# Performance work log

Hardware: AMD Instinct MI355X
Metric: run time of the kernel (lower is better)

The kernel has to match this reference:

```python
import jax, jax.numpy as jnp
import numpy as np

# SqueezeSeg CRF config
NUM_CLASS = 4
SIZE_Z, SIZE_A = 3, 5            # LCN_HEIGHT, LCN_WIDTH
B, H, W = 16, 64, 512            # batch, zenith, azimuth
RCRF_ITER = 3
BI_FILTER_COEF = 0.1
ANG_FILTER_COEF = 0.02
ANG_THETA_A = 0.9
BILATERAL_THETA_A = 0.9
K = SIZE_Z * SIZE_A              # 15 -> 14 neighbors (center excluded)

# neighbor offsets of the 3x5 condensing kernel, center excluded
OFFSETS = [(dz, da) for dz in range(SIZE_Z) for da in range(SIZE_A)
           if not (dz == SIZE_Z // 2 and da == SIZE_A // 2)]

def _gauss_weights(theta_sq):
    # angular_filter_kernel: Gaussian of squared spatial offset, center zeroed
    g = [np.exp(-((dz - SIZE_Z // 2) ** 2 + (da - SIZE_A // 2) ** 2) / (2.0 * theta_sq))
         for dz, da in OFFSETS]
    return jnp.asarray(np.array(g, dtype=np.float32))

def gather_neighbors(x):
    # x: [B,C,H,W] -> [B,C,K-1,H,W]; zero-padded 'same' neighborhood gather
    pz, pa = SIZE_Z // 2, SIZE_A // 2
    xp = jnp.pad(x, ((0, 0), (0, 0), (pz, pz), (pa, pa)))
    return jnp.stack([xp[:, :, dz:dz + H, da:da + W] for dz, da in OFFSETS], axis=2)

def setup_inputs() -> dict:
    key = jax.random.key(0)
    k1, k2, k3 = jax.random.split(key, 3)
    x = jax.random.normal(k1, (B, NUM_CLASS, H, W), dtype=jnp.float32)
    bilateral_filters = jax.random.uniform(k2, (B, 1, K - 1, H, W), dtype=jnp.float32)
    lidar_mask = (jax.random.uniform(k3, (B, 1, H, W)) > 0.5).astype(jnp.float32)
    return {"x": x, "bilateral_filters": bilateral_filters, "lidar_mask": lidar_mask}

def reference(x, bilateral_filters, lidar_mask):
    g_ang = _gauss_weights(ANG_THETA_A ** 2)
    g_bi = _gauss_weights(BILATERAL_THETA_A ** 2)
    compat = jnp.ones((NUM_CLASS, NUM_CLASS), jnp.float32) - jnp.eye(NUM_CLASS, dtype=jnp.float32)
    ang_compat = compat * ANG_FILTER_COEF   # [out_class, in_class] 1x1 conv
    bi_compat = compat * BI_FILTER_COEF

    for _ in range(RCRF_ITER):
        unary = jax.nn.softmax(x, axis=1)                     # softmax over class dim
        nb = gather_neighbors(unary)                          # [B,C,14,H,W]
        # depthwise angular filters = Gaussian-weighted neighbor sums
        ang = jnp.einsum('k,bckhw->bchw', g_ang, nb)
        bi_ang = jnp.einsum('k,bckhw->bchw', g_bi, nb)
        # condensing conv on masked unary, weighted by per-pixel bilateral filters
        nb_m = gather_neighbors(unary * lidar_mask)           # [B,C,14,H,W]
        condensed = jnp.sum(nb_m * bilateral_filters, axis=2) # [B,C,H,W]
        bi = condensed * lidar_mask * bi_ang
        # 1x1 compatibility transforms
        ang2 = jnp.einsum('oc,bchw->bohw', ang_compat, ang)
        bi2 = jnp.einsum('oc,bchw->bohw', bi_compat, bi)
        x = unary + ang2 + bi2
    return x
```

## Files before the change

kernel.cpp:

```cpp
#include <hip/hip_runtime.h>


#define NCLASS 4
#define HH 64
#define WW 512
#define BB 16
#define TH 8
#define TW 64
#define UR (TH + 6)
#define UC (TW + 12)
#define PLANE (HH * WW)

#define G1 0.53940412f
#define G2 0.29095687f
#define G4 0.08466190f
#define G5 0.04566227f

#define TAPS                                                                 \
    const int   DZ[14] = {-1,-1,-1,-1,-1,  0, 0, 0, 0,  1, 1, 1, 1, 1};      \
    const int   DA[14] = {-2,-1, 0, 1, 2, -2,-1, 1, 2, -2,-1, 0, 1, 2};      \
    const float GW[14] = {G5,G2,G1,G2,G5, G4,G1,G1,G4, G5,G2,G1,G2,G5};

template <int MR, int MC, bool FINAL>
__device__ __forceinline__ void crf_step(
    float4 (*__restrict__ u_lds)[UC], const float (*__restrict__ m_lds)[UC],
    const float* __restrict__ filt, float* __restrict__ dst,
    int b, int h0, int w0, int tid)
{
    constexpr int RH = TH + 2 * MR;
    constexpr int RW = TW + 2 * MC;
    constexpr int NS = (RH * RW + 255) / 256;
    TAPS

    float4 xnew[NS];

#pragma unroll
    for (int j = 0; j < NS; ++j) {
        const int s = tid + 256 * j;
        float4 r = make_float4(0.f, 0.f, 0.f, 0.f);
        if (s < RH * RW) {
            const int lr = s / RW;
            const int lc = s - lr * RW;
            const int gh = h0 + lr - MR;
            const int gw = w0 + lc - MC;
            const int ur = lr + (3 - MR);
            const int uc = lc + (6 - MC);
            if (gh >= 0 && gh < HH && gw >= 0 && gw < WW) {
                float a0 = 0.f, a1 = 0.f, a2 = 0.f, a3 = 0.f;
                float c0 = 0.f, c1 = 0.f, c2 = 0.f, c3 = 0.f;
                const float mcen = m_lds[ur][uc];
                const float* fp = filt + ((size_t)b * 14 * HH + gh) * WW + gw;
#pragma unroll
                for (int k = 0; k < 14; ++k) {
                    const float  f  = fp[(size_t)k * PLANE];
                    const float  mn = m_lds[ur + DZ[k]][uc + DA[k]];
                    const float4 u  = u_lds[ur + DZ[k]][uc + DA[k]];
                    const float  fm = f * mn;
                    const float  gk = GW[k];
                    a0 = fmaf(gk, u.x, a0);  c0 = fmaf(fm, u.x, c0);
                    a1 = fmaf(gk, u.y, a1);  c1 = fmaf(fm, u.y, c1);
                    a2 = fmaf(gk, u.z, a2);  c2 = fmaf(fm, u.z, c2);
                    a3 = fmaf(gk, u.w, a3);  c3 = fmaf(fm, u.w, c3);
                }
                const float b0 = c0 * mcen * a0;
                const float b1 = c1 * mcen * a1;
                const float b2 = c2 * mcen * a2;
                const float b3 = c3 * mcen * a3;
                const float sa = a0 + a1 + a2 + a3;
                const float sb = b0 + b1 + b2 + b3;
                const float4 ucen = u_lds[ur][uc];
                r.x = ucen.x + 0.02f * (sa - a0) + 0.1f * (sb - b0);
                r.y = ucen.y + 0.02f * (sa - a1) + 0.1f * (sb - b1);
                r.z = ucen.z + 0.02f * (sa - a2) + 0.1f * (sb - b2);
                r.w = ucen.w + 0.02f * (sa - a3) + 0.1f * (sb - b3);
                if (!FINAL) {
                    const float mx  = fmaxf(fmaxf(r.x, r.y), fmaxf(r.z, r.w));
                    const float e0  = __expf(r.x - mx);
                    const float e1  = __expf(r.y - mx);
                    const float e2  = __expf(r.z - mx);
                    const float e3  = __expf(r.w - mx);
                    const float inv = 1.0f / (e0 + e1 + e2 + e3);
                    r = make_float4(e0 * inv, e1 * inv, e2 * inv, e3 * inv);
                }
            }
            if (FINAL) {
                float* o = dst + ((size_t)b * NCLASS * HH + gh) * WW + gw;
                o[0]         = r.x;
                o[PLANE]     = r.y;
                o[2 * PLANE] = r.z;
                o[3 * PLANE] = r.w;
            }
        }
        if (!FINAL) xnew[j] = r;
    }

    if (!FINAL) {
        __syncthreads();
#pragma unroll
        for (int j = 0; j < NS; ++j) {
            const int s = tid + 256 * j;
            if (s < RH * RW) {
                const int lr = s / RW;
                const int lc = s - lr * RW;
                u_lds[lr + (3 - MR)][lc + (6 - MC)] = xnew[j];
            }
        }
        __syncthreads();
    }
}

__global__ __launch_bounds__(256, 4) void crf_fused(
    const float* __restrict__ xin,
    const float* __restrict__ filt,
    const float* __restrict__ mask,
    float* __restrict__ xout)
{
    __shared__ float4 u_lds[UR][UC];
    __shared__ float  m_lds[UR][UC];

    const int b   = blockIdx.z;
    const int h0  = blockIdx.y * TH;
    const int w0  = blockIdx.x * TW;
    const int tid = threadIdx.x;

    for (int idx = tid; idx < UR * UC; idx += 256) {
        const int lr = idx / UC;
        const int lc = idx - lr * UC;
        const int gh = h0 + lr - 3;
        const int gw = w0 + lc - 6;
        float4 u = make_float4(0.f, 0.f, 0.f, 0.f);
        float  m = 0.f;
        if (gh >= 0 && gh < HH && gw >= 0 && gw < WW) {
            const float* px = xin + ((size_t)b * NCLASS * HH + gh) * WW + gw;
            const float v0 = px[0];
            const float v1 = px[PLANE];
            const float v2 = px[2 * PLANE];
            const float v3 = px[3 * PLANE];
            const float mx = fmaxf(fmaxf(v0, v1), fmaxf(v2, v3));
            const float e0 = __expf(v0 - mx);
            const float e1 = __expf(v1 - mx);
            const float e2 = __expf(v2 - mx);
            const float e3 = __expf(v3 - mx);
            const float inv = 1.0f / (e0 + e1 + e2 + e3);
            u = make_float4(e0 * inv, e1 * inv, e2 * inv, e3 * inv);
            m = mask[((size_t)b * HH + gh) * WW + gw];
        }
        u_lds[lr][lc] = u;
        m_lds[lr][lc] = m;
    }
    __syncthreads();

    crf_step<2, 4, false>(u_lds, m_lds, filt, xout, b, h0, w0, tid);
    crf_step<1, 2, false>(u_lds, m_lds, filt, xout, b, h0, w0, tid);
    crf_step<0, 0, true >(u_lds, m_lds, filt, xout, b, h0, w0, tid);
}

extern "C" void kernel_launch(void* const* d_in, const int* in_sizes, int n_in,
                              void* d_out, int out_size, void* d_ws, size_t ws_size,
                              hipStream_t stream) {
    const float* x    = (const float*)d_in[0];
    const float* filt = (const float*)d_in[1];
    const float* msk  = (const float*)d_in[2];
    float* out = (float*)d_out;
    (void)d_ws; (void)ws_size;

    dim3 grid(WW / TW, HH / TH, BB);
    dim3 block(256);
    crf_fused<<<grid, block, 0, stream>>>(x, filt, msk, out);
}
```

Measured before the change: 98.66 us.

## Process two adjacent pixels per thread with swizzled LDS and vectorized loads

Each thread now computes two horizontally adjacent pixels. Each stencil row of six LDS values is loaded once and shared by both outputs, which reduces LDS reads per pixel. The bilateral filter, input and mask loads and the output stores become float2 accesses. LDS columns are swizzled (even/odd split) so that threads reading pairs avoid bank conflicts. The cost is higher register pressure from the 28 filter values and doubled accumulators, which may reduce occupancy, and odd-width halo regions need extra edge-handling branches.

```diff
diff --git a/kernel.cpp b/kernel.cpp
--- a/kernel.cpp
+++ b/kernel.cpp
@@ -9,6 +9,7 @@
 #define TW 64
 #define UR (TH + 6)
 #define UC (TW + 12)
+#define UCH (UC / 2)
 #define PLANE (HH * WW)
 
 #define G1 0.53940412f
@@ -16,10 +17,24 @@
 #define G4 0.08466190f
 #define G5 0.04566227f
 
-#define TAPS                                                                 \
-    const int   DZ[14] = {-1,-1,-1,-1,-1,  0, 0, 0, 0,  1, 1, 1, 1, 1};      \
-    const int   DA[14] = {-2,-1, 0, 1, 2, -2,-1, 1, 2, -2,-1, 0, 1, 2};      \
-    const float GW[14] = {G5,G2,G1,G2,G5, G4,G1,G1,G4, G5,G2,G1,G2,G5};
+__device__ __forceinline__ constexpr int swz(int c) {
+    return (c & 1) * UCH + (c >> 1);
+}
+
+__device__ __forceinline__ constexpr int tapk(int dz, int da) {
+    const int idx = (dz + 1) * 5 + (da + 2);
+    return idx > 7 ? idx - 1 : idx;
+}
+
+__device__ __forceinline__ float4 softmax4(float4 v) {
+    const float mx = fmaxf(fmaxf(v.x, v.y), fmaxf(v.z, v.w));
+    const float e0 = __expf(v.x - mx);
+    const float e1 = __expf(v.y - mx);
+    const float e2 = __expf(v.z - mx);
+    const float e3 = __expf(v.w - mx);
+    const float inv = 1.0f / (e0 + e1 + e2 + e3);
+    return make_float4(e0 * inv, e1 * inv, e2 * inv, e3 * inv);
+}
 
 template <int MR, int MC, bool FINAL>
 __device__ __forceinline__ void crf_step(
@@ -27,82 +42,143 @@
     const float* __restrict__ filt, float* __restrict__ dst,
     int b, int h0, int w0, int tid)
 {
-    constexpr int RH = TH + 2 * MR;
-    constexpr int RW = TW + 2 * MC;
-    constexpr int NS = (RH * RW + 255) / 256;
-    TAPS
-
-    float4 xnew[NS];
+    constexpr int RH  = TH + 2 * MR;
+    constexpr int RW  = TW + 2 * MC;
+    constexpr int NPX = RH * RW;
+    constexpr int NS  = (NPX + 511) / 512;
+    const float GW[14] = {G5,G2,G1,G2,G5, G4,G1,G1,G4, G5,G2,G1,G2,G5};
+
+    float4 xn[NS][2];
 
 #pragma unroll
     for (int j = 0; j < NS; ++j) {
-        const int s = tid + 256 * j;
-        float4 r = make_float4(0.f, 0.f, 0.f, 0.f);
-        if (s < RH * RW) {
+        xn[j][0] = make_float4(0.f, 0.f, 0.f, 0.f);
+        xn[j][1] = make_float4(0.f, 0.f, 0.f, 0.f);
+        const int s = 2 * (tid + 256 * j);
+        if (s < NPX) {
             const int lr = s / RW;
             const int lc = s - lr * RW;
             const int gh = h0 + lr - MR;
             const int gw = w0 + lc - MC;
             const int ur = lr + (3 - MR);
             const int uc = lc + (6 - MC);
-            if (gh >= 0 && gh < HH && gw >= 0 && gw < WW) {
-                float a0 = 0.f, a1 = 0.f, a2 = 0.f, a3 = 0.f;
-                float c0 = 0.f, c1 = 0.f, c2 = 0.f, c3 = 0.f;
-                const float mcen = m_lds[ur][uc];
-                const float* fp = filt + ((size_t)b * 14 * HH + gh) * WW + gw;
+            const bool rowIn = (gh >= 0) && (gh < HH);
+            const bool in0 = rowIn && (gw >= 0) && (gw < WW);
+            const bool in1 = rowIn && (gw + 1 >= 0) && (gw + 1 < WW);
+
+            float F0[14], F1[14];
+            const float* fp = filt + ((size_t)b * 14 * HH + gh) * WW + gw;
+            if (in0 && in1) {
 #pragma unroll
                 for (int k = 0; k < 14; ++k) {
-                    const float  f  = fp[(size_t)k * PLANE];
-                    const float  mn = m_lds[ur + DZ[k]][uc + DA[k]];
-                    const float4 u  = u_lds[ur + DZ[k]][uc + DA[k]];
-                    const float  fm = f * mn;
-                    const float  gk = GW[k];
-                    a0 = fmaf(gk, u.x, a0);  c0 = fmaf(fm, u.x, c0);
-                    a1 = fmaf(gk, u.y, a1);  c1 = fmaf(fm, u.y, c1);
-                    a2 = fmaf(gk, u.z, a2);  c2 = fmaf(fm, u.z, c2);
-                    a3 = fmaf(gk, u.w, a3);  c3 = fmaf(fm, u.w, c3);
-                }
-                const float b0 = c0 * mcen * a0;
-                const float b1 = c1 * mcen * a1;
-                const float b2 = c2 * mcen * a2;
-                const float b3 = c3 * mcen * a3;
-                const float sa = a0 + a1 + a2 + a3;
-                const float sb = b0 + b1 + b2 + b3;
-                const float4 ucen = u_lds[ur][uc];
-                r.x = ucen.x + 0.02f * (sa - a0) + 0.1f * (sb - b0);
-                r.y = ucen.y + 0.02f * (sa - a1) + 0.1f * (sb - b1);
-                r.z = ucen.z + 0.02f * (sa - a2) + 0.1f * (sb - b2);
-                r.w = ucen.w + 0.02f * (sa - a3) + 0.1f * (sb - b3);
-                if (!FINAL) {
-                    const float mx  = fmaxf(fmaxf(r.x, r.y), fmaxf(r.z, r.w));
-                    const float e0  = __expf(r.x - mx);
-                    const float e1  = __expf(r.y - mx);
-                    const float e2  = __expf(r.z - mx);
-                    const float e3  = __expf(r.w - mx);
-                    const float inv = 1.0f / (e0 + e1 + e2 + e3);
-                    r = make_float4(e0 * inv, e1 * inv, e2 * inv, e3 * inv);
-                }
-            }
+                    const float2 f2 = *(const float2*)(fp + (size_t)k * PLANE);
+                    F0[k] = f2.x; F1[k] = f2.y;
+                }
+            } else {
+#pragma unroll
+                for (int k = 0; k < 14; ++k) {
+                    F0[k] = in0 ? fp[(size_t)k * PLANE] : 0.f;
+                    F1[k] = in1 ? fp[(size_t)k * PLANE + 1] : 0.f;
+                }
+            }
+
+            float4 A0 = make_float4(0.f,0.f,0.f,0.f), C0 = A0, A1 = A0, C1 = A0;
+            float4 cen0, cen1;
+            float  mc0 = 0.f, mc1 = 0.f;
+#pragma unroll
+            for (int dz = -1; dz <= 1; ++dz) {
+                const int rr = ur + dz;
+                float4 U[6];
+                float  M[6];
+#pragma unroll
+                for (int t = 0; t < 6; ++t) {
+                    const int col = uc - 2 + t;
+                    U[t] = u_lds[rr][swz(col)];
+                    M[t] = m_lds[rr][swz(col)];
+                }
+                if (dz == 0) {
+                    cen0 = U[2]; cen1 = U[3];
+                    mc0  = M[2]; mc1  = M[3];
+                }
+#pragma unroll
+                for (int da = -2; da <= 2; ++da) {
+                    if (dz == 0 && da == 0) continue;
+                    const int   k   = tapk(dz, da);
+                    const float gk  = GW[k];
+                    const float fm0 = F0[k] * M[da + 2];
+                    const float fm1 = F1[k] * M[da + 3];
+                    const float4 u0 = U[da + 2];
+                    const float4 u1 = U[da + 3];
+                    A0.x = fmaf(gk,  u0.x, A0.x);  C0.x = fmaf(fm0, u0.x, C0.x);
+                    A0.y = fmaf(gk,  u0.y, A0.y);  C0.y = fmaf(fm0, u0.y, C0.y);
+                    A0.z = fmaf(gk,  u0.z, A0.z);  C0.z = fmaf(fm0, u0.z, C0.z);
+                    A0.w = fmaf(gk,  u0.w, A0.w);  C0.w = fmaf(fm0, u0.w, C0.w);
+                    A1.x = fmaf(gk,  u1.x, A1.x);  C1.x = fmaf(fm1, u1.x, C1.x);
+                    A1.y = fmaf(gk,  u1.y, A1.y);  C1.y = fmaf(fm1, u1.y, C1.y);
+                    A1.z = fmaf(gk,  u1.z, A1.z);  C1.z = fmaf(fm1, u1.z, C1.z);
+                    A1.w = fmaf(gk,  u1.w, A1.w);  C1.w = fmaf(fm1, u1.w, C1.w);
+                }
+            }
+
+            const float b0x = C0.x * mc0 * A0.x;
+            const float b0y = C0.y * mc0 * A0.y;
+            const float b0z = C0.z * mc0 * A0.z;
+            const float b0w = C0.w * mc0 * A0.w;
+            const float b1x = C1.x * mc1 * A1.x;
+            const float b1y = C1.y * mc1 * A1.y;
+            const float b1z = C1.z * mc1 * A1.z;
+            const float b1w = C1.w * mc1 * A1.w;
+            const float sa0 = A0.x + A0.y + A0.z + A0.w;
+            const float sb0 = b0x + b0y + b0z + b0w;
+            const float sa1 = A1.x + A1.y + A1.z + A1.w;
+            const float sb1 = b1x + b1y + b1z + b1w;
+            float4 r0, r1;
+            r0.x = cen0.x + 0.02f * (sa0 - A0.x) + 0.1f * (sb0 - b0x);
+            r0.y = cen0.y + 0.02f * (sa0 - A0.y) + 0.1f * (sb0 - b0y);
+            r0.z = cen0.z + 0.02f * (sa0 - A0.z) + 0.1f * (sb0 - b0z);
+            r0.w = cen0.w + 0.02f * (sa0 - A0.w) + 0.1f * (sb0 - b0w);
+            r1.x = cen1.x + 0.02f * (sa1 - A1.x) + 0.1f * (sb1 - b1x);
+            r1.y = cen1.y + 0.02f * (sa1 - A1.y) + 0.1f * (sb1 - b1y);
+            r1.z = cen1.z + 0.02f * (sa1 - A1.z) + 0.1f * (sb1 - b1z);
+            r1.w = cen1.w + 0.02f * (sa1 - A1.w) + 0.1f * (sb1 - b1w);
+
             if (FINAL) {
                 float* o = dst + ((size_t)b * NCLASS * HH + gh) * WW + gw;
-                o[0]         = r.x;
-                o[PLANE]     = r.y;
-                o[2 * PLANE] = r.z;
-                o[3 * PLANE] = r.w;
+                if (in0 && in1) {
+                    *(float2*)(o)             = make_float2(r0.x, r1.x);
+                    *(float2*)(o +     PLANE) = make_float2(r0.y, r1.y);
+                    *(float2*)(o + 2 * PLANE) = make_float2(r0.z, r1.z);
+                    *(float2*)(o + 3 * PLANE) = make_float2(r0.w, r1.w);
+                } else {
+                    if (in0) {
+                        o[0] = r0.x; o[PLANE] = r0.y;
+                        o[2 * PLANE] = r0.z; o[3 * PLANE] = r0.w;
+                    }
+                    if (in1) {
+                        o[1] = r1.x; o[PLANE + 1] = r1.y;
+                        o[2 * PLANE + 1] = r1.z; o[3 * PLANE + 1] = r1.w;
+                    }
+                }
+            } else {
+                if (in0) xn[j][0] = softmax4(r0);
+                if (in1) xn[j][1] = softmax4(r1);
             }
         }
-        if (!FINAL) xnew[j] = r;
     }
 
     if (!FINAL) {
         __syncthreads();
 #pragma unroll
         for (int j = 0; j < NS; ++j) {
-            const int s = tid + 256 * j;
-            if (s < RH * RW) {
+            const int s = 2 * (tid + 256 * j);
+            if (s < NPX) {
                 const int lr = s / RW;
                 const int lc = s - lr * RW;
-                u_lds[lr + (3 - MR)][lc + (6 - MC)] = xnew[j];
+                const int ur = lr + (3 - MR);
+                const int uc = lc + (6 - MC);
+                float4 (*uw)[UC] = (float4 (*)[UC])u_lds;
+                uw[ur][swz(uc)]     = xn[j][0];
+                uw[ur][swz(uc + 1)] = xn[j][1];
             }
         }
         __syncthreads();
@@ -123,30 +199,48 @@
     const int w0  = blockIdx.x * TW;
     const int tid = threadIdx.x;
 
-    for (int idx = tid; idx < UR * UC; idx += 256) {
-        const int lr = idx / UC;
-        const int lc = idx - lr * UC;
-        const int gh = h0 + lr - 3;
-        const int gw = w0 + lc - 6;
-        float4 u = make_float4(0.f, 0.f, 0.f, 0.f);
-        float  m = 0.f;
-        if (gh >= 0 && gh < HH && gw >= 0 && gw < WW) {
-            const float* px = xin + ((size_t)b * NCLASS * HH + gh) * WW + gw;
-            const float v0 = px[0];
-            const float v1 = px[PLANE];
-            const float v2 = px[2 * PLANE];
-            const float v3 = px[3 * PLANE];
-            const float mx = fmaxf(fmaxf(v0, v1), fmaxf(v2, v3));
-            const float e0 = __expf(v0 - mx);
-            const float e1 = __expf(v1 - mx);
-            const float e2 = __expf(v2 - mx);
-            const float e3 = __expf(v3 - mx);
-            const float inv = 1.0f / (e0 + e1 + e2 + e3);
-            u = make_float4(e0 * inv, e1 * inv, e2 * inv, e3 * inv);
-            m = mask[((size_t)b * HH + gh) * WW + gw];
+#pragma unroll
+    for (int j = 0; j < 3; ++j) {
+        const int s = 2 * (tid + 256 * j);
+        if (s < UR * UC) {
+            const int lr = s / UC;
+            const int lc = s - lr * UC;
+            const int gh = h0 + lr - 3;
+            const int gw = w0 + lc - 6;
+            const bool rowIn = (gh >= 0) && (gh < HH);
+            const bool in0 = rowIn && (gw >= 0) && (gw < WW);
+            const bool in1 = rowIn && (gw + 1 >= 0) && (gw + 1 < WW);
+            float4 u0 = make_float4(0.f,0.f,0.f,0.f);
+            float4 u1 = u0;
+            float  m0 = 0.f, m1 = 0.f;
+            if (in0 && in1) {
+                const float* px = xin  + ((size_t)b * NCLASS * HH + gh) * WW + gw;
+                const float* mp = mask + ((size_t)b * HH + gh) * WW + gw;
+                const float2 v0 = *(const float2*)(px);
+                const float2 v1 = *(const float2*)(px +     PLANE);
+                const float2 v2 = *(const float2*)(px + 2 * PLANE);
+                const float2 v3 = *(const float2*)(px + 3 * PLANE);
+                const float2 mm = *(const float2*)(mp);
+                u0 = softmax4(make_float4(v0.x, v1.x, v2.x, v3.x));
+                u1 = softmax4(make_float4(v0.y, v1.y, v2.y, v3.y));
+                m0 = mm.x; m1 = mm.y;
+            } else {
+                if (in0) {
+                    const float* px = xin + ((size_t)b * NCLASS * HH + gh) * WW + gw;
+                    u0 = softmax4(make_float4(px[0], px[PLANE], px[2*PLANE], px[3*PLANE]));
+                    m0 = mask[((size_t)b * HH + gh) * WW + gw];
+                }
+                if (in1) {
+                    const float* px = xin + ((size_t)b * NCLASS * HH + gh) * WW + gw + 1;
+                    u1 = softmax4(make_float4(px[0], px[PLANE], px[2*PLANE], px[3*PLANE]));
+                    m1 = mask[((size_t)b * HH + gh) * WW + gw + 1];
+                }
+            }
+            u_lds[lr][swz(lc)]     = u0;
+            u_lds[lr][swz(lc + 1)] = u1;
+            m_lds[lr][swz(lc)]     = m0;
+            m_lds[lr][swz(lc + 1)] = m1;
         }
-        u_lds[lr][lc] = u;
-        m_lds[lr][lc] = m;
     }
     __syncthreads();
 
```

After: 131.6 us. 33.4% more time.

## Register-block 4 rows per thread with separable Gaussian and LDS ping-pong buffers

Applied to the files above, without the earlier changes.

Each thread now computes a vertical strip of 4 output pixels. Every loaded neighbor row is reused across up to 3 outputs, and the angular Gaussian is evaluated separably (horizontal sum, then vertical weighting), which cuts LDS reads and FMAs. Double-buffering the unary tile in LDS removes the extra barrier and register staging between CRF iterations. The cost is more LDS per block (occupancy hint lowered from 4 to 3), higher register pressure, and fewer active threads in later steps.

```diff
diff --git a/kernel.cpp b/kernel.cpp
--- a/kernel.cpp
+++ b/kernel.cpp
@@ -7,115 +7,163 @@
 #define BB 16
 #define TH 8
 #define TW 64
-#define UR (TH + 6)
-#define UC (TW + 12)
+#define UR 14
+#define UC 76
 #define PLANE (HH * WW)
 
 #define G1 0.53940412f
-#define G2 0.29095687f
 #define G4 0.08466190f
-#define G5 0.04566227f
-
-#define TAPS                                                                 \
-    const int   DZ[14] = {-1,-1,-1,-1,-1,  0, 0, 0, 0,  1, 1, 1, 1, 1};      \
-    const int   DA[14] = {-2,-1, 0, 1, 2, -2,-1, 1, 2, -2,-1, 0, 1, 2};      \
-    const float GW[14] = {G5,G2,G1,G2,G5, G4,G1,G1,G4, G5,G2,G1,G2,G5};
-
-template <int MR, int MC, bool FINAL>
+
+__device__ __forceinline__ constexpr int tapk(int dz, int da) {
+    const int idx = (dz + 1) * 5 + (da + 2);
+    return idx > 7 ? idx - 1 : idx;
+}
+
+__device__ __forceinline__ float4 softmax4(float4 v) {
+    const float mx = fmaxf(fmaxf(v.x, v.y), fmaxf(v.z, v.w));
+    const float e0 = __expf(v.x - mx);
+    const float e1 = __expf(v.y - mx);
+    const float e2 = __expf(v.z - mx);
+    const float e3 = __expf(v.w - mx);
+    const float inv = 1.0f / (e0 + e1 + e2 + e3);
+    return make_float4(e0 * inv, e1 * inv, e2 * inv, e3 * inv);
+}
+
+template <int PT0, int PT1, int PC0, int PC1, bool FINAL>
 __device__ __forceinline__ void crf_step(
-    float4 (*__restrict__ u_lds)[UC], const float (*__restrict__ m_lds)[UC],
-    const float* __restrict__ filt, float* __restrict__ dst,
+    const float4 (*__restrict__ u_src)[UC],
+    float4 (*__restrict__ u_dst)[UC],
+    const float (*__restrict__ m_lds)[UC],
+    const float* __restrict__ filt,
+    float* __restrict__ out,
     int b, int h0, int w0, int tid)
 {
-    constexpr int RH = TH + 2 * MR;
-    constexpr int RW = TW + 2 * MC;
-    constexpr int NS = (RH * RW + 255) / 256;
-    TAPS
-
-    float4 xnew[NS];
-
-#pragma unroll
-    for (int j = 0; j < NS; ++j) {
-        const int s = tid + 256 * j;
-        float4 r = make_float4(0.f, 0.f, 0.f, 0.f);
-        if (s < RH * RW) {
-            const int lr = s / RW;
-            const int lc = s - lr * RW;
-            const int gh = h0 + lr - MR;
-            const int gw = w0 + lc - MC;
-            const int ur = lr + (3 - MR);
-            const int uc = lc + (6 - MC);
-            if (gh >= 0 && gh < HH && gw >= 0 && gw < WW) {
-                float a0 = 0.f, a1 = 0.f, a2 = 0.f, a3 = 0.f;
-                float c0 = 0.f, c1 = 0.f, c2 = 0.f, c3 = 0.f;
-                const float mcen = m_lds[ur][uc];
-                const float* fp = filt + ((size_t)b * 14 * HH + gh) * WW + gw;
-#pragma unroll
-                for (int k = 0; k < 14; ++k) {
-                    const float  f  = fp[(size_t)k * PLANE];
-                    const float  mn = m_lds[ur + DZ[k]][uc + DA[k]];
-                    const float4 u  = u_lds[ur + DZ[k]][uc + DA[k]];
-                    const float  fm = f * mn;
-                    const float  gk = GW[k];
-                    a0 = fmaf(gk, u.x, a0);  c0 = fmaf(fm, u.x, c0);
-                    a1 = fmaf(gk, u.y, a1);  c1 = fmaf(fm, u.y, c1);
-                    a2 = fmaf(gk, u.z, a2);  c2 = fmaf(fm, u.z, c2);
-                    a3 = fmaf(gk, u.w, a3);  c3 = fmaf(fm, u.w, c3);
+    constexpr int RH    = PT1 - PT0 + 1;
+    constexpr int RW    = PC1 - PC0 + 1;
+    constexpr int QR    = (RH + 3) / 4;
+    constexpr int SLOTS = QR * RW;
+    static_assert(SLOTS <= 256, "one pass only");
+
+    if (tid < SLOTS) {
+        const int qr    = tid / RW;
+        const int c     = tid - qr * RW;
+        const int pcol  = PC0 + c;
+        const int prow0 = PT0 + qr * 4;
+        const int gw    = w0 + pcol - 6;
+        const bool colIn = (gw >= 0) && (gw < WW);
+
+        bool valid[4];
+        int  ghr[4];
+#pragma unroll
+        for (int i = 0; i < 4; ++i) {
+            const int pr = prow0 + i;
+            const int gh = h0 + pr - 3;
+            ghr[i]   = gh;
+            valid[i] = (pr <= PT1) && colIn && (gh >= 0) && (gh < HH);
+        }
+
+        float4 A[4], C[4], cen[4];
+        float  mcen[4];
+#pragma unroll
+        for (int i = 0; i < 4; ++i) {
+            A[i] = make_float4(0.f, 0.f, 0.f, 0.f);
+            C[i] = A[i]; cen[i] = A[i]; mcen[i] = 0.f;
+        }
+
+        const float* fbase = filt + (size_t)b * 14 * PLANE;
+
+#pragma unroll
+        for (int ir = 0; ir < 6; ++ir) {
+            const int prin = prow0 - 1 + ir;
+            if (prin <= PT1 + 1) {
+                float4 U[5];
+                float  M[5];
+#pragma unroll
+                for (int t = 0; t < 5; ++t) {
+                    U[t] = u_src[prin][pcol - 2 + t];
+                    M[t] = m_lds[prin][pcol - 2 + t];
                 }
-                const float b0 = c0 * mcen * a0;
-                const float b1 = c1 * mcen * a1;
-                const float b2 = c2 * mcen * a2;
-                const float b3 = c3 * mcen * a3;
-                const float sa = a0 + a1 + a2 + a3;
-                const float sb = b0 + b1 + b2 + b3;
-                const float4 ucen = u_lds[ur][uc];
-                r.x = ucen.x + 0.02f * (sa - a0) + 0.1f * (sb - b0);
-                r.y = ucen.y + 0.02f * (sa - a1) + 0.1f * (sb - b1);
-                r.z = ucen.z + 0.02f * (sa - a2) + 0.1f * (sb - b2);
-                r.w = ucen.w + 0.02f * (sa - a3) + 0.1f * (sb - b3);
-                if (!FINAL) {
-                    const float mx  = fmaxf(fmaxf(r.x, r.y), fmaxf(r.z, r.w));
-                    const float e0  = __expf(r.x - mx);
-                    const float e1  = __expf(r.y - mx);
-                    const float e2  = __expf(r.z - mx);
-                    const float e3  = __expf(r.w - mx);
-                    const float inv = 1.0f / (e0 + e1 + e2 + e3);
-                    r = make_float4(e0 * inv, e1 * inv, e2 * inv, e3 * inv);
+                float4 S;
+                S.x = fmaf(G4, U[0].x + U[4].x, fmaf(G1, U[1].x + U[3].x, U[2].x));
+                S.y = fmaf(G4, U[0].y + U[4].y, fmaf(G1, U[1].y + U[3].y, U[2].y));
+                S.z = fmaf(G4, U[0].z + U[4].z, fmaf(G1, U[1].z + U[3].z, U[2].z));
+                S.w = fmaf(G4, U[0].w + U[4].w, fmaf(G1, U[1].w + U[3].w, U[2].w));
+
+#pragma unroll
+                for (int i = 0; i < 4; ++i) {
+                    const int dz = ir - 1 - i;
+                    if (dz < -1 || dz > 1) continue;
+                    const float gz = (dz == 0) ? 1.0f : G1;
+                    A[i].x = fmaf(gz, S.x, A[i].x);
+                    A[i].y = fmaf(gz, S.y, A[i].y);
+                    A[i].z = fmaf(gz, S.z, A[i].z);
+                    A[i].w = fmaf(gz, S.w, A[i].w);
+                    if (dz == 0) { cen[i] = U[2]; mcen[i] = M[2]; }
+                    if (valid[i]) {
+                        const float* fp = fbase + (size_t)ghr[i] * WW + gw;
+#pragma unroll
+                        for (int da = -2; da <= 2; ++da) {
+                            if (dz == 0 && da == 0) continue;
+                            const int   k  = tapk(dz, da);
+                            const float f  = fp[(size_t)k * PLANE];
+                            const float fm = f * M[da + 2];
+                            C[i].x = fmaf(fm, U[da + 2].x, C[i].x);
+                            C[i].y = fmaf(fm, U[da + 2].y, C[i].y);
+                            C[i].z = fmaf(fm, U[da + 2].z, C[i].z);
+                            C[i].w = fmaf(fm, U[da + 2].w, C[i].w);
+                        }
+                    }
                 }
             }
+        }
+
+#pragma unroll
+        for (int i = 0; i < 4; ++i) {
+            const int pr = prow0 + i;
+            if (pr > PT1) continue;
+            float4 r = make_float4(0.f, 0.f, 0.f, 0.f);
+            if (valid[i]) {
+                float4 Aa;
+                Aa.x = A[i].x - cen[i].x;
+                Aa.y = A[i].y - cen[i].y;
+                Aa.z = A[i].z - cen[i].z;
+                Aa.w = A[i].w - cen[i].w;
+                const float bx = C[i].x * mcen[i] * Aa.x;
+                const float by = C[i].y * mcen[i] * Aa.y;
+                const float bz = C[i].z * mcen[i] * Aa.z;
+                const float bw = C[i].w * mcen[i] * Aa.w;
+                const float sa = Aa.x + Aa.y + Aa.z + Aa.w;
+                const float sb = bx + by + bz + bw;
+                r.x = cen[i].x + 0.02f * (sa - Aa.x) + 0.1f * (sb - bx);
+                r.y = cen[i].y + 0.02f * (sa - Aa.y) + 0.1f * (sb - by);
+                r.z = cen[i].z + 0.02f * (sa - Aa.z) + 0.1f * (sb - bz);
+                r.w = cen[i].w + 0.02f * (sa - Aa.w) + 0.1f * (sb - bw);
+            }
             if (FINAL) {
-                float* o = dst + ((size_t)b * NCLASS * HH + gh) * WW + gw;
-                o[0]         = r.x;
-                o[PLANE]     = r.y;
-                o[2 * PLANE] = r.z;
-                o[3 * PLANE] = r.w;
+                if (valid[i]) {
+                    float* o = out + ((size_t)b * NCLASS * HH + ghr[i]) * WW + gw;
+                    o[0]         = r.x;
+                    o[PLANE]     = r.y;
+                    o[2 * PLANE] = r.z;
+                    o[3 * PLANE] = r.w;
+                }
+            } else {
+                u_dst[pr][pcol] = valid[i] ? softmax4(r)
+                                           : make_float4(0.f, 0.f, 0.f, 0.f);
             }
         }
-        if (!FINAL) xnew[j] = r;
     }
-
-    if (!FINAL) {
-        __syncthreads();
-#pragma unroll
-        for (int j = 0; j < NS; ++j) {
-            const int s = tid + 256 * j;
-            if (s < RH * RW) {
-                const int lr = s / RW;
-                const int lc = s - lr * RW;
-                u_lds[lr + (3 - MR)][lc + (6 - MC)] = xnew[j];
-            }
-        }
-        __syncthreads();
-    }
-}
-
-__global__ __launch_bounds__(256, 4) void crf_fused(
+    if (!FINAL) __syncthreads();
+}
+
+__global__ __launch_bounds__(256, 3) void crf_fused(
     const float* __restrict__ xin,
     const float* __restrict__ filt,
     const float* __restrict__ mask,
     float* __restrict__ xout)
 {
-    __shared__ float4 u_lds[UR][UC];
+    __shared__ float4 uA[UR][UC];
+    __shared__ float4 uB[UR][UC];
     __shared__ float  m_lds[UR][UC];
 
     const int b   = blockIdx.z;
@@ -132,27 +180,17 @@
         float  m = 0.f;
         if (gh >= 0 && gh < HH && gw >= 0 && gw < WW) {
             const float* px = xin + ((size_t)b * NCLASS * HH + gh) * WW + gw;
-            const float v0 = px[0];
-            const float v1 = px[PLANE];
-            const float v2 = px[2 * PLANE];
-            const float v3 = px[3 * PLANE];
-            const float mx = fmaxf(fmaxf(v0, v1), fmaxf(v2, v3));
-            const float e0 = __expf(v0 - mx);
-            const float e1 = __expf(v1 - mx);
-            const float e2 = __expf(v2 - mx);
-            const float e3 = __expf(v3 - mx);
-            const float inv = 1.0f / (e0 + e1 + e2 + e3);
-            u = make_float4(e0 * inv, e1 * inv, e2 * inv, e3 * inv);
+            u = softmax4(make_float4(px[0], px[PLANE], px[2 * PLANE], px[3 * PLANE]));
             m = mask[((size_t)b * HH + gh) * WW + gw];
         }
-        u_lds[lr][lc] = u;
+        uA[lr][lc]    = u;
         m_lds[lr][lc] = m;
     }
     __syncthreads();
 
-    crf_step<2, 4, false>(u_lds, m_lds, filt, xout, b, h0, w0, tid);
-    crf_step<1, 2, false>(u_lds, m_lds, filt, xout, b, h0, w0, tid);
-    crf_step<0, 0, true >(u_lds, m_lds, filt, xout, b, h0, w0, tid);
+    crf_step<1, 12, 2, 73, false>(uA, uB, m_lds, filt, xout, b, h0, w0, tid);
+    crf_step<2, 11, 4, 71, false>(uB, uA, m_lds, filt, xout, b, h0, w0, tid);
+    crf_step<3, 10, 6, 69, true >(uA, uB, m_lds, filt, xout, b, h0, w0, tid);
 }
 
 extern "C" void kernel_launch(void* const* d_in, const int* in_sizes, int n_in,
```

Result: slower. 110.3 us (+11.7%).
